# Kernel optimization log

Hardware: AMD Instinct MI355X
Metric: run time of the kernel (lower is better)

## Reference

```python
import jax, jax.numpy as jnp
import numpy as np

B, L, IN_DIM = 1024, 2048, 64
ATT_DIM, H, TOPK = 64, 4, 64
D = ATT_DIM // H  # head_dim = 16
SCALE = D ** 0.5


def setup_inputs() -> dict:
    key = jax.random.key(0)
    k1, k2, k3, k4, k5, k6, k7 = jax.random.split(key, 7)
    return {
        "target_item": jax.random.normal(k1, (B, IN_DIM), dtype=jnp.float32),
        "item_sequence": jax.random.normal(k2, (B, L, IN_DIM), dtype=jnp.float32),
        "mask": jax.random.randint(k3, (B, L), 0, 2, dtype=jnp.int32),
        # Linear weights stored as (in, out); x @ W == torch Linear(x)
        "W_q": jax.random.normal(k4, (IN_DIM, ATT_DIM), dtype=jnp.float32) * 0.05,
        "W_h": jax.random.normal(k5, (IN_DIM, ATT_DIM), dtype=jnp.float32) * 0.05,
        "W_v": jax.random.normal(k6, (IN_DIM, ATT_DIM), dtype=jnp.float32) * 0.05,
        "W_o": jax.random.normal(k7, (ATT_DIM, IN_DIM), dtype=jnp.float32) * 0.05,
    }


def reference(target_item, item_sequence, mask, W_q, W_h, W_v, W_o):
    b = target_item.shape[0]
    # Projections (Kc == 0 path: item_feat_seq == item_sequence)
    q = (target_item @ W_q).reshape(b, H, D)          # b h d (single query)
    k = (item_sequence @ W_h).reshape(b, L, H, D)      # b l h d
    v = (item_sequence @ W_v).reshape(b, L, H, D)      # b l h d

    scores = jnp.einsum("bhd,blhd->bhl", q, k) / SCALE  # b h l
    scores = jnp.where(mask[:, None, :] == 0, jnp.float32(-1e9), scores)

    topk_scores, topk_idx = jax.lax.top_k(scores, TOPK)  # b h k
    # gather the top-k value vectors: v -> b h l d, gather along l
    v_bhld = jnp.transpose(v, (0, 2, 1, 3))              # b h l d
    topk_value = jnp.take_along_axis(v_bhld, topk_idx[..., None], axis=2)  # b h k d

    attn = jax.nn.softmax(topk_scores, axis=-1)          # b h k
    out = jnp.einsum("bhk,bhkd->bhd", attn, topk_value)  # b h d
    out = out.reshape(b, H * D) @ W_o                    # b x input_dim
    return out
```

## Files before the change

### kernel.cpp

```cpp
#include <hip/hip_runtime.h>

#define B_   1024
#define L_   2048
#define IND_ 64
#define H_   4
#define K_   64

__global__ __launch_bounds__(64) void prep_weff_k(const float* __restrict__ target,
                                                  const float* __restrict__ Wq,
                                                  const float* __restrict__ Wh,
                                                  float* __restrict__ weff) {
  const int b = blockIdx.x;
  const int t = threadIdx.x;
  __shared__ float tgt[64];
  __shared__ double q[64];
  tgt[t] = target[b * 64 + t];
  __syncthreads();
  double acc = 0.0;
#pragma unroll
  for (int j = 0; j < 64; ++j) acc += (double)tgt[j] * (double)Wq[j * 64 + t];
  q[t] = acc;
  __syncthreads();
#pragma unroll
  for (int h = 0; h < H_; ++h) {
    double a2 = 0.0;
#pragma unroll
    for (int d = 0; d < 16; ++d) a2 += q[h * 16 + d] * (double)Wh[t * 64 + h * 16 + d];
    weff[((size_t)b * H_ + h) * 64 + t] = (float)(a2 * 0.25);
  }
}

__device__ __forceinline__ unsigned f2key(float s) {
  unsigned u = __float_as_uint(s);
  return (u & 0x80000000u) ? ~u : (u | 0x80000000u);
}
__device__ __forceinline__ float key2f(unsigned k) {
  unsigned u = (k & 0x80000000u) ? (k & 0x7FFFFFFFu) : ~k;
  return __uint_as_float(u);
}

template <int CTRL>
__device__ __forceinline__ float dpp_f(float x) {
  return __int_as_float(
      __builtin_amdgcn_update_dpp(0, __float_as_int(x), CTRL, 0xf, 0xf, true));
}
template <int OFF>
__device__ __forceinline__ float swz_f(float x) {
  return __int_as_float(__builtin_amdgcn_ds_swizzle(__float_as_int(x), OFF));
}

__global__ __launch_bounds__(256, 4) void attn_main_k(const float* __restrict__ seq,
                                                      const int* __restrict__ mask,
                                                      const float* __restrict__ weff,
                                                      const float* __restrict__ Wv,
                                                      const float* __restrict__ Wo,
                                                      float* __restrict__ out) {
  __shared__ float scores[L_ * H_];
  __shared__ int   sidx[H_][K_];
  __shared__ float sw[H_][K_];
  __shared__ float svec[H_][64];
  __shared__ float tvec[H_][16];
  __shared__ float part[H_][64];

  const int b = blockIdx.x;
  const int tid = threadIdx.x;
  const int w = tid >> 6;
  const int ln = tid & 63;
  const int g = ln >> 4;
  const int j = ln & 15;
  const float* __restrict__ seqb = seq + (size_t)b * (L_ * IND_);
  const int* __restrict__ maskb = mask + (size_t)b * L_;
  const bool b1 = (ln & 1) != 0;
  const bool b2 = (ln & 2) != 0;

  float wefv[H_][4];
  {
    const float* wp = weff + (size_t)b * (H_ * 64) + (j << 2);
#pragma unroll
    for (int h = 0; h < H_; ++h) {
      const float4 v = *reinterpret_cast<const float4*>(wp + (h << 6));
      wefv[h][0] = v.x; wefv[h][1] = v.y; wefv[h][2] = v.z; wefv[h][3] = v.w;
    }
  }

  const float4* __restrict__ lp4 =
      reinterpret_cast<const float4*>(seqb) + (w << 6) + (g << 4) + j;
  const int rb0 = (w << 2) + g;

  float4 vvA[8], vvB[8];

#define LOADB(V, SB)                                                          \
  {                                                                           \
    _Pragma("unroll") for (int u = 0; u < 8; ++u)                             \
        V[u] = lp4[(((SB) << 3) + u) << 8];                                   \
  }
#define COMPUTE(V, SB)                                                        \
  {                                                                           \
    _Pragma("unroll") for (int u = 0; u < 8; ++u) {                           \
      const int s = ((SB) << 3) + u;                                          \
      const float4 v = V[u];                                                  \
      float p0 = v.x * wefv[0][0]; p0 = fmaf(v.y, wefv[0][1], p0);            \
      p0 = fmaf(v.z, wefv[0][2], p0); p0 = fmaf(v.w, wefv[0][3], p0);         \
      float p1 = v.x * wefv[1][0]; p1 = fmaf(v.y, wefv[1][1], p1);            \
      p1 = fmaf(v.z, wefv[1][2], p1); p1 = fmaf(v.w, wefv[1][3], p1);         \
      float p2 = v.x * wefv[2][0]; p2 = fmaf(v.y, wefv[2][1], p2);            \
      p2 = fmaf(v.z, wefv[2][2], p2); p2 = fmaf(v.w, wefv[2][3], p2);         \
      float p3 = v.x * wefv[3][0]; p3 = fmaf(v.y, wefv[3][1], p3);            \
      p3 = fmaf(v.z, wefv[3][2], p3); p3 = fmaf(v.w, wefv[3][3], p3);         \
                       \
      const float a  = (b1 ? p1 : p0) + dpp_f<0xB1>(b1 ? p0 : p1);            \
      const float bb = (b1 ? p3 : p2) + dpp_f<0xB1>(b1 ? p2 : p3);            \
      float c = (b2 ? bb : a) + dpp_f<0x4E>(b2 ? a : bb);                     \
      c += swz_f<0x101F>(c);                                       \
      c += swz_f<0x201F>(c);                                       \
      const int row = (s << 4) + rb0;                                         \
      if (j < 4) scores[(row << 2) + j] = c;                                  \
    }                                                                         \
  }

  LOADB(vvA, 0);
  LOADB(vvB, 1);  COMPUTE(vvA, 0);
  LOADB(vvA, 2);  COMPUTE(vvB, 1);
  LOADB(vvB, 3);  COMPUTE(vvA, 2);
  LOADB(vvA, 4);  COMPUTE(vvB, 3);
  LOADB(vvB, 5);  COMPUTE(vvA, 4);
  LOADB(vvA, 6);  COMPUTE(vvB, 5);
  LOADB(vvB, 7);  COMPUTE(vvA, 6);
  LOADB(vvA, 8);  COMPUTE(vvB, 7);
  LOADB(vvB, 9);  COMPUTE(vvA, 8);
  LOADB(vvA, 10); COMPUTE(vvB, 9);
  LOADB(vvB, 11); COMPUTE(vvA, 10);
  LOADB(vvA, 12); COMPUTE(vvB, 11);
  LOADB(vvB, 13); COMPUTE(vvA, 12);
  LOADB(vvA, 14); COMPUTE(vvB, 13);
  LOADB(vvB, 15); COMPUTE(vvA, 14);
                  COMPUTE(vvB, 15);
#undef LOADB
#undef COMPUTE

  unsigned mbits = 0;
#pragma unroll
  for (int t = 0; t < 32; ++t) mbits |= (maskb[(t << 6) + ln] ? 1u : 0u) << t;

  __syncthreads();

  unsigned kk[32];
  const unsigned KNEG = f2key(-1e9f);
#pragma unroll
  for (int t = 0; t < 32; ++t) {
    const float s_ = scores[(((t << 6) + ln) << 2) + w];
    kk[t] = ((mbits >> t) & 1u) ? f2key(s_) : KNEG;
  }

  unsigned kmax = 0u;
#pragma unroll
  for (int q = 0; q < 32; ++q) kmax = max(kmax, kk[q]);
#pragma unroll
  for (int off = 32; off >= 1; off >>= 1)
    kmax = max(kmax, (unsigned)__shfl_xor((int)kmax, off, 64));
  const float smax = key2f(kmax);

  unsigned lo = 0u, hi = 0xFFFFFFFFu;
  while (lo < hi) {
    const unsigned span = hi - lo;
    const unsigned mid = lo + (span >> 1) + (span & 1u);
    int c = 0;
#pragma unroll
    for (int q = 0; q < 32; ++q) c += (kk[q] >= mid) ? 1 : 0;
#pragma unroll
    for (int off = 32; off >= 1; off >>= 1) c += __shfl_xor(c, off, 64);
    if (c >= K_) lo = mid; else hi = mid - 1;
  }
  const unsigned V = lo;
  int cg = 0;
#pragma unroll
  for (int q = 0; q < 32; ++q) cg += (kk[q] > V) ? 1 : 0;
#pragma unroll
  for (int off = 32; off >= 1; off >>= 1) cg += __shfl_xor(cg, off, 64);
  const int m = K_ - cg;

  {
    const unsigned long long lmlt = (1ull << ln) - 1ull;
    int gbase = 0, etaken = 0;
#pragma unroll
    for (int q = 0; q < 32; ++q) {
      const unsigned key = kk[q];
      const int l = ln + (q << 6);
      const bool gt = key > V;
      const bool eq = key == V;
      const unsigned long long bgt = __ballot(gt);
      const unsigned long long beq = __ballot(eq);
      if (gt) {
        const int pos = gbase + __popcll(bgt & lmlt);
        sidx[w][pos] = l;
        sw[w][pos] = expf(key2f(key) - smax);
      }
      const int navail = __popcll(beq);
      const int take = min(m - etaken, navail);
      if (eq) {
        const int rk = __popcll(beq & lmlt);
        if (rk < take) {
          const int pos = 63 - (etaken + rk);
          sidx[w][pos] = l;
          sw[w][pos] = expf(key2f(key) - smax);
        }
      }
      gbase += __popcll(bgt);
      etaken += take;
    }
  }

  {
    const int cg4 = ln & 15;
    const int rg = ln >> 4;
    float4 sv = make_float4(0.f, 0.f, 0.f, 0.f);
    float z = 0.f;
#pragma unroll
    for (int q = 0; q < 16; ++q) {
      const int sl = (q << 2) + rg;
      const int idx = sidx[w][sl];
      const float wt = sw[w][sl];
      const float4 v =
          *reinterpret_cast<const float4*>(seqb + (size_t)idx * 64 + (cg4 << 2));
      sv.x = fmaf(wt, v.x, sv.x);
      sv.y = fmaf(wt, v.y, sv.y);
      sv.z = fmaf(wt, v.z, sv.z);
      sv.w = fmaf(wt, v.w, sv.w);
      z += wt;
    }
#pragma unroll
    for (int off = 16; off <= 32; off <<= 1) {
      sv.x += __shfl_xor(sv.x, off, 64);
      sv.y += __shfl_xor(sv.y, off, 64);
      sv.z += __shfl_xor(sv.z, off, 64);
      sv.w += __shfl_xor(sv.w, off, 64);
      z += __shfl_xor(z, off, 64);
    }
    if (rg == 0) {
      const float inv = 1.f / z;
      svec[w][(cg4 << 2) + 0] = sv.x * inv;
      svec[w][(cg4 << 2) + 1] = sv.y * inv;
      svec[w][(cg4 << 2) + 2] = sv.z * inv;
      svec[w][(cg4 << 2) + 3] = sv.w * inv;
    }
  }

  {
    float tp = 0.f;
#pragma unroll
    for (int i16 = 0; i16 < 16; ++i16) {
      const int i = (i16 << 2) + g;
      tp = fmaf(svec[w][i], Wv[i * 64 + (w << 4) + j], tp);
    }
    tp += __shfl_xor(tp, 16, 64);
    tp += __shfl_xor(tp, 32, 64);
    if (ln < 16) tvec[w][ln] = tp;
    float o = 0.f;
#pragma unroll
    for (int d = 0; d < 16; ++d)
      o = fmaf(tvec[w][d], Wo[((w << 4) + d) * 64 + ln], o);
    part[w][ln] = o;
  }
  __syncthreads();
  if (tid < 64)
    out[(size_t)b * 64 + tid] = part[0][tid] + part[1][tid] + part[2][tid] + part[3][tid];
}

extern "C" void kernel_launch(void* const* d_in, const int* in_sizes, int n_in,
                              void* d_out, int out_size, void* d_ws, size_t ws_size,
                              hipStream_t stream) {
  const float* target = (const float*)d_in[0];
  const float* seq    = (const float*)d_in[1];
  const int*   mask   = (const int*)d_in[2];
  const float* Wq     = (const float*)d_in[3];
  const float* Wh     = (const float*)d_in[4];
  const float* Wv     = (const float*)d_in[5];
  const float* Wo     = (const float*)d_in[6];
  float* out  = (float*)d_out;
  float* weff = (float*)d_ws;

  prep_weff_k<<<B_, 64, 0, stream>>>(target, Wq, Wh, weff);
  attn_main_k<<<B_, 256, 0, stream>>>(seq, mask, weff, Wv, Wo, out);
}
```

Measured before the change: 125.0 us.

## Fuse effective-weight prep into main attention kernel, overlapping with first loads

Removes the separate prep kernel and computes the per-head effective key weights inside each wave of the main kernel using wave shuffles. The computation sits after the first two sequence tile loads are issued, so the double-precision work can overlap memory latency. This drops one kernel launch and the workspace round trip. In exchange each of the four waves recomputes the same 64x64 and 64x16 products in fp64, adding ALU work and shuffles per block.

```diff
diff --git a/kernel.cpp b/kernel.cpp
--- a/kernel.cpp
+++ b/kernel.cpp
@@ -6,30 +6,6 @@
 #define H_   4
 #define K_   64
 
-__global__ __launch_bounds__(64) void prep_weff_k(const float* __restrict__ target,
-                                                  const float* __restrict__ Wq,
-                                                  const float* __restrict__ Wh,
-                                                  float* __restrict__ weff) {
-  const int b = blockIdx.x;
-  const int t = threadIdx.x;
-  __shared__ float tgt[64];
-  __shared__ double q[64];
-  tgt[t] = target[b * 64 + t];
-  __syncthreads();
-  double acc = 0.0;
-#pragma unroll
-  for (int j = 0; j < 64; ++j) acc += (double)tgt[j] * (double)Wq[j * 64 + t];
-  q[t] = acc;
-  __syncthreads();
-#pragma unroll
-  for (int h = 0; h < H_; ++h) {
-    double a2 = 0.0;
-#pragma unroll
-    for (int d = 0; d < 16; ++d) a2 += q[h * 16 + d] * (double)Wh[t * 64 + h * 16 + d];
-    weff[((size_t)b * H_ + h) * 64 + t] = (float)(a2 * 0.25);
-  }
-}
-
 __device__ __forceinline__ unsigned f2key(float s) {
   unsigned u = __float_as_uint(s);
   return (u & 0x80000000u) ? ~u : (u | 0x80000000u);
@@ -49,9 +25,11 @@
   return __int_as_float(__builtin_amdgcn_ds_swizzle(__float_as_int(x), OFF));
 }
 
-__global__ __launch_bounds__(256, 4) void attn_main_k(const float* __restrict__ seq,
+__global__ __launch_bounds__(256, 4) void attn_main_k(const float* __restrict__ target,
+                                                      const float* __restrict__ seq,
                                                       const int* __restrict__ mask,
-                                                      const float* __restrict__ weff,
+                                                      const float* __restrict__ Wq,
+                                                      const float* __restrict__ Wh,
                                                       const float* __restrict__ Wv,
                                                       const float* __restrict__ Wo,
                                                       float* __restrict__ out) {
@@ -72,16 +50,6 @@
   const int* __restrict__ maskb = mask + (size_t)b * L_;
   const bool b1 = (ln & 1) != 0;
   const bool b2 = (ln & 2) != 0;
-
-  float wefv[H_][4];
-  {
-    const float* wp = weff + (size_t)b * (H_ * 64) + (j << 2);
-#pragma unroll
-    for (int h = 0; h < H_; ++h) {
-      const float4 v = *reinterpret_cast<const float4*>(wp + (h << 6));
-      wefv[h][0] = v.x; wefv[h][1] = v.y; wefv[h][2] = v.z; wefv[h][3] = v.w;
-    }
-  }
 
   const float4* __restrict__ lp4 =
       reinterpret_cast<const float4*>(seqb) + (w << 6) + (g << 4) + j;
@@ -119,7 +87,36 @@
   }
 
   LOADB(vvA, 0);
-  LOADB(vvB, 1);  COMPUTE(vvA, 0);
+  LOADB(vvB, 1);
+
+  float wefv[H_][4];
+  {
+    const float tgtv = target[b * 64 + ln];
+    double qa = 0.0;
+#pragma unroll
+    for (int jj = 0; jj < 64; ++jj) {
+      const double tj = (double)__shfl(tgtv, jj, 64);
+      qa = fma(tj, (double)Wq[jj * 64 + ln], qa);
+    }
+    float wef_i[H_];
+#pragma unroll
+    for (int h = 0; h < H_; ++h) {
+      double a2 = 0.0;
+#pragma unroll
+      for (int d = 0; d < 16; ++d) {
+        const double qv = __shfl(qa, h * 16 + d, 64);
+        a2 = fma(qv, (double)Wh[ln * 64 + h * 16 + d], a2);
+      }
+      wef_i[h] = (float)(a2 * 0.25);
+    }
+#pragma unroll
+    for (int h = 0; h < H_; ++h)
+#pragma unroll
+      for (int e = 0; e < 4; ++e)
+        wefv[h][e] = __shfl(wef_i[h], (j << 2) + e, 64);
+  }
+
+                  COMPUTE(vvA, 0);
   LOADB(vvA, 2);  COMPUTE(vvB, 1);
   LOADB(vvB, 3);  COMPUTE(vvA, 2);
   LOADB(vvA, 4);  COMPUTE(vvB, 3);
@@ -276,9 +273,8 @@
   const float* Wh     = (const float*)d_in[4];
   const float* Wv     = (const float*)d_in[5];
   const float* Wo     = (const float*)d_in[6];
-  float* out  = (float*)d_out;
-  float* weff = (float*)d_ws;
-
-  prep_weff_k<<<B_, 64, 0, stream>>>(target, Wq, Wh, weff);
-  attn_main_k<<<B_, 256, 0, stream>>>(seq, mask, weff, Wv, Wo, out);
-}
+  float* out = (float*)d_out;
+  (void)d_ws; (void)ws_size;
+
+  attn_main_k<<<B_, 256, 0, stream>>>(target, seq, mask, Wq, Wh, Wv, Wo, out);
+}
```

Result: faster. 122.1 us (-2.3%).
